# Performance work log

Measured on AMD Instinct MI355X. Metric: run time of the kernel, lower is better.

Reference implementation:

```python
import jax, jax.numpy as jnp
import numpy as np

B = 32          # batch size
N = 32          # image dim -> P = N*N points per sample
P = N * N
F = 64          # point feature dim (= MLP output)
K = 32          # max_neighbors
R = 0.1         # ball-query radius
EPS = 1e-5      # batchnorm eps


def setup_inputs() -> dict:
    key = jax.random.key(0)
    ks = jax.random.split(key, 4)
    NP = B * P
    x = jax.random.normal(ks[0], (NP, F), jnp.float32)
    pos = jax.random.uniform(ks[1], (NP, 2), jnp.float32)
    # module requires exactly N*N points per sample, sorted by batch
    batch = jnp.repeat(jnp.arange(B, dtype=jnp.int32), P)
    # MLP([66,128,64]) params: Linear->BN->ReLU->Linear
    W1 = jax.random.normal(ks[2], (F + 2, 128), jnp.float32) * (1.0 / np.sqrt(F + 2))
    b1 = jnp.zeros((128,), jnp.float32)
    gamma1 = jnp.ones((128,), jnp.float32)
    beta1 = jnp.zeros((128,), jnp.float32)
    W2 = jax.random.normal(ks[3], (128, F), jnp.float32) * (1.0 / np.sqrt(128))
    b2 = jnp.zeros((F,), jnp.float32)
    return {"x": x, "pos": pos, "batch": batch, "W1": W1, "b1": b1,
            "gamma1": gamma1, "beta1": beta1, "W2": W2, "b2": b2}


def reference(x, pos, batch, W1, b1, gamma1, beta1, W2, b2):
    NP = x.shape[0]
    posb = pos.reshape(B, P, 2)
    # pixel (target) index of every query point: batch*N*N + row*N + col
    rows = jnp.clip((pos[:, 1] * N).astype(jnp.int32), 0, N - 1)
    cols = jnp.clip((pos[:, 0] * N).astype(jnp.int32), 0, N - 1)
    pix = batch.astype(jnp.int32) * (N * N) + rows * N + cols          # [NP]
    # radius ball query within each batch sample (deterministic: nearest-K within R)
    d2 = jnp.sum((posb[:, :, None, :] - posb[:, None, :, :]) ** 2, -1)  # [B,P,P]
    d2 = jnp.where(d2 <= R * R, d2, jnp.inf)
    negd, nbr = jax.lax.top_k(-d2, K)                                   # [B,P,K]
    valid = jnp.isfinite(negd)
    src = (jnp.arange(B, dtype=jnp.int32)[:, None, None] * P + nbr).reshape(-1)  # [B*P*K]
    dst = jnp.broadcast_to(pix.reshape(B, P)[:, :, None], (B, P, K)).reshape(-1)
    mask = valid.reshape(-1) & (src != dst)          # remove_self_loops
    # PointNetConv message: concat(x_j, pos_j - pos_i); pos_i indexed by mapped target
    relpos = pos[src] - pos[dst]
    msg_nb = jnp.concatenate([x[src], relpos], -1)                    # [B*P*K, F+2]
    # add_self_loops: edge (i, i) for every node -> relpos = 0
    msg_self = jnp.concatenate([x, jnp.zeros_like(pos)], -1)          # [NP, F+2]
    msg = jnp.concatenate([msg_nb, msg_self], 0)
    m = jnp.concatenate([mask, jnp.ones((NP,), bool)], 0)
    tgt = jnp.concatenate([dst, jnp.arange(NP, dtype=jnp.int32)], 0)
    # MLP: Linear -> BatchNorm(training stats over valid messages) -> ReLU -> Linear
    z = msg @ W1 + b1
    mf = m.astype(z.dtype)[:, None]
    cnt = jnp.sum(mf)
    mean = jnp.sum(z * mf, 0, keepdims=True) / cnt
    var = jnp.sum(((z - mean) ** 2) * mf, 0, keepdims=True) / cnt
    h = jax.nn.relu((z - mean) / jnp.sqrt(var + EPS) * gamma1 + beta1)
    o = h @ W2 + b2                                                    # [M, F]
    # scatter-max aggregation into B*N*N pixel nodes (self loops make all nonempty)
    o = jnp.where(m[:, None], o, -jnp.inf)
    pixel_features = jax.ops.segment_max(o, tgt, num_segments=NP)
    images = pixel_features.reshape(B, N, N, F).transpose(0, 3, 1, 2)
    return images
```

## Files before the change

### kernel.cpp

```cpp
#include <hip/hip_runtime.h>
#include <hip/hip_bf16.h>
#include <hip/hip_fp16.h>
#include <math.h>


#define NPTS   32768
#define KNB    32
#define BN_EPS 1e-5f

#define WS_NBRS     0u
#define WS_NBRCNT   4194304u
#define WS_SCSH     4719616u
#define WS_W2B      4720640u
#define WS_PART     4737024u
#define WS_Y        5265408u
#define WS_SCRATCH  5265408u
#define WS_WB       13654016u
#define WS_QCNT     22042624u
#define WS_QSTART   22173696u
#define WS_QLIST    22304768u
#define WS_ISLOT    22435840u
#define WS_SELF     22566912u
#define WS_SHP      30955520u
#define WS_BQPART   22566912u

typedef __attribute__((ext_vector_type(8))) _Float16 half8;
typedef __attribute__((ext_vector_type(2))) _Float16 half2v;
typedef __attribute__((ext_vector_type(4))) float floatx4;

__device__ __forceinline__ unsigned short f2h_bits(float f) {
    _Float16 h = (_Float16)f;
    return *reinterpret_cast<unsigned short*>(&h);
}
__device__ __forceinline__ float bf_lo(unsigned int w) { return __uint_as_float(w << 16); }
__device__ __forceinline__ float bf_hi(unsigned int w) { return __uint_as_float(w & 0xffff0000u); }
__device__ __forceinline__ unsigned int pack_bf2(float lo, float hi) {
    __hip_bfloat162 hh = __float22bfloat162_rn(make_float2(lo, hi));
    return *reinterpret_cast<unsigned int*>(&hh);
}
__device__ __forceinline__ unsigned int pack_h2(float lo, float hi) {
    half2v hh = { (_Float16)lo, (_Float16)hi };
    return *reinterpret_cast<unsigned int*>(&hh);
}

union ShBQ {
    struct {
        float2 poss[1024];
        float accd[1024], accx[1024], accy[1024];
        unsigned long long cand[4][256];
    } bq;
    struct {
        int cntS[1024], preS[1024], offS[1024], pixOf[1024];
        int wtot[4];
    } pm;
};

__launch_bounds__(256)
__global__ void k_bq(const float* __restrict__ pos,
                     int* __restrict__ nbrs, int* __restrict__ nbr_cnt,
                     float* __restrict__ bqpart,
                     const float* __restrict__ W2, unsigned short* __restrict__ w2b,
                     int* __restrict__ qcnt, int* __restrict__ qstart,
                     int* __restrict__ qlist, int* __restrict__ islot) {
    __shared__ ShBQ sh;
    int tid = threadIdx.x;

    if (blockIdx.x < 32) {
        int s = blockIdx.x;
        int gt = s * 256 + tid;
        {
            int j  = gt & 7;
            int L  = (gt >> 3) & 63;
            int ks = (gt >> 9) & 3;
            int t4 = gt >> 11;
            int k = ks * 32 + (L >> 4) * 8 + j;
            int n = t4 * 16 + (L & 15);
            w2b[gt] = f2h_bits(W2[k * 64 + n]);
        }
        int base = s << 10;
        for (int i = tid; i < 1024; i += 256) sh.pm.cntS[i] = 0;
        __syncthreads();
        for (int ql = tid; ql < 1024; ql += 256) {
            float2 p = *(const float2*)&pos[2 * (base + ql)];
            int row = min(max((int)(p.y * 32.0f), 0), 31);
            int col = min(max((int)(p.x * 32.0f), 0), 31);
            int pixl = row * 32 + col;
            sh.pm.pixOf[ql] = pixl;
            atomicAdd(&sh.pm.cntS[pixl], 1);
        }
        __syncthreads();
        int a0 = sh.pm.cntS[4 * tid], a1 = sh.pm.cntS[4 * tid + 1];
        int a2 = sh.pm.cntS[4 * tid + 2], a3 = sh.pm.cntS[4 * tid + 3];
        int tsum = a0 + a1 + a2 + a3;
        int lane = tid & 63, wv = tid >> 6;
        int v = tsum;
        for (int o = 1; o < 64; o <<= 1) { int u = __shfl_up(v, o); if (lane >= o) v += u; }
        if (lane == 63) sh.pm.wtot[wv] = v;
        __syncthreads();
        int wbase = 0;
        for (int w = 0; w < wv; ++w) wbase += sh.pm.wtot[w];
        int excl = wbase + v - tsum;
        sh.pm.preS[4 * tid] = excl;
        sh.pm.preS[4 * tid + 1] = excl + a0;
        sh.pm.preS[4 * tid + 2] = excl + a0 + a1;
        sh.pm.preS[4 * tid + 3] = excl + a0 + a1 + a2;
        __syncthreads();
        for (int i = tid; i < 1024; i += 256) sh.pm.offS[i] = sh.pm.preS[i];
        __syncthreads();
        for (int ql = tid; ql < 1024; ql += 256) {
            int p = sh.pm.pixOf[ql];
            int slot = atomicAdd(&sh.pm.offS[p], 1);
            qlist[base + slot] = base + ql;
            islot[base + ql] = base + slot;
        }
        for (int i = tid; i < 1024; i += 256) {
            qcnt[base + i] = sh.pm.cntS[i];
            qstart[base + i] = base + sh.pm.preS[i];
        }
        return;
    }

    int bqid = blockIdx.x - 32;
    int wave = tid >> 6, lane = tid & 63;
    int s = bqid >> 5;
    int chunk = bqid & 31;
    int base = s << 10;
    for (int i = tid; i < 1024; i += 256) sh.bq.poss[i] = *(const float2*)&pos[2 * (base + i)];
    for (int i = tid; i < 1024; i += 256) { sh.bq.accd[i] = 0.0f; sh.bq.accx[i] = 0.0f; sh.bq.accy[i] = 0.0f; }
    __syncthreads();
    float2 pr[16];
#pragma unroll
    for (int k = 0; k < 16; ++k) pr[k] = sh.bq.poss[k * 64 + lane];
    unsigned long long lb = (1ull << lane) - 1ull;

    float aD = 0, aE = 0, aF = 0;
    for (int qi = 0; qi < 8; ++qi) {
        int ql = chunk * 32 + wave * 8 + qi;
        int q = base + ql;
        float2 qp = sh.bq.poss[ql];
        int row = min(max((int)(qp.y * 32.0f), 0), 31);
        int col = min(max((int)(qp.x * 32.0f), 0), 31);
        int pixl = row * 32 + col;
        float2 tp = sh.bq.poss[pixl];
        int cnt = 0;
        __builtin_amdgcn_wave_barrier();
#pragma unroll
        for (int k = 0; k < 16; ++k) {
            float dx = pr[k].x - qp.x, dy = pr[k].y - qp.y;
            float d2 = __fadd_rn(__fmul_rn(dx, dx), __fmul_rn(dy, dy));
            bool pred = (d2 <= 0.01f);
            unsigned long long mask = __ballot(pred);
            if (pred) {
                int slot = cnt + (int)__popcll(mask & lb);
                if (slot < 256)
                    sh.bq.cand[wave][slot] = ((unsigned long long)__float_as_uint(d2) << 32)
                                             | (unsigned int)(k * 64 + lane);
            }
            cnt += (int)__popcll(mask);
        }
        cnt = min(cnt, 256);
        __builtin_amdgcn_wave_barrier();
        int osel = 0;
        for (int cb = 0; cb < cnt; cb += 64) {
            int i = cb + lane;
            bool sel = false;
            int j = 0;
            if (i < cnt) {
                unsigned long long key = sh.bq.cand[wave][i];
                j = (int)(key & 0xffffffffu);
                if (cnt <= KNB) {
                    sel = (j != pixl);
                } else {
                    int rank = 0;
                    for (int t = 0; t < cnt; ++t) rank += (sh.bq.cand[wave][t] < key) ? 1 : 0;
                    sel = (rank < KNB) && (j != pixl);
                }
            }
            unsigned long long mask = __ballot(sel);
            if (sel) {
                int slot = osel + (int)__popcll(mask & lb);
                nbrs[q * KNB + slot] = base + j;
                float rx = sh.bq.poss[j].x - tp.x, ry = sh.bq.poss[j].y - tp.y;
                aD += rx * rx; aE += rx * ry; aF += ry * ry;
                atomicAdd(&sh.bq.accd[j], 1.0f);
                atomicAdd(&sh.bq.accx[j], tp.x);
                atomicAdd(&sh.bq.accy[j], tp.y);
            }
            osel += (int)__popcll(mask);
        }
        if (lane == 0) nbr_cnt[q] = osel;
    }
#pragma unroll
    for (int o = 1; o < 64; o <<= 1) {
        aD += __shfl_xor(aD, o); aE += __shfl_xor(aE, o); aF += __shfl_xor(aF, o);
    }
    __syncthreads();
    float* pb = &bqpart[bqid * 3076];
    for (int i = tid; i < 1024; i += 256) {
        pb[i] = sh.bq.accd[i]; pb[1024 + i] = sh.bq.accx[i]; pb[2048 + i] = sh.bq.accy[i];
    }
    if (tid == 0) { pb[3072] = aD; pb[3073] = aE; pb[3074] = aF; }
}

__launch_bounds__(512)
__global__ void k_y(const float* __restrict__ x, const float* __restrict__ W1,
                    const float* __restrict__ b1, const float* __restrict__ pos,
                    const float* __restrict__ bqpart,
                    unsigned int* __restrict__ yb, float* __restrict__ partials) {
    __shared__ float w1s[64 * 128];
    __shared__ float stage[8][512];
    __shared__ float lsum[515];
    __shared__ float degS[128], stxS[128], styS[128];
    int tid = threadIdx.x;
    int nblock = blockIdx.x * 128;
    for (int i = tid; i < 64 * 128; i += 512) w1s[i] = W1[i];
    for (int i = tid; i < 515; i += 512) lsum[i] = 0.0f;
    if (tid < 128) {
        int n = nblock + tid;
        int s = n >> 10, off = n & 1023;
        const float* pb = &bqpart[(s * 32) * 3076];
        float d = 0, xx = 0, yy = 0;
        for (int j = 0; j < 32; ++j) {
            d  += pb[j * 3076 + off];
            xx += pb[j * 3076 + 1024 + off];
            yy += pb[j * 3076 + 2048 + off];
        }
        degS[tid] = d; stxS[tid] = xx; styS[tid] = yy;
    }
    __syncthreads();
    int wave = tid >> 6, lane = tid & 63;
    int f0 = 2 * lane, f1 = 2 * lane + 1;
    float b10 = b1[f0], b11 = b1[f1];
    float* st = &stage[wave][0];
    float P0 = 0, Q0 = 0, R0 = 0, S0 = 0, P1 = 0, Q1 = 0, R1 = 0, S1 = 0;
    float sB = 0, sC = 0, sDeg = 0;

    for (int it = 0; it < 2; ++it) {
        int nbase = nblock + (wave * 2 + it) * 8;
        __builtin_amdgcn_wave_barrier();
#pragma unroll
        for (int mm = 0; mm < 8; ++mm)
            st[mm * 64 + lane] = x[(nbase + mm) * 64 + lane];
        __builtin_amdgcn_wave_barrier();
        float z0[8], z1[8];
#pragma unroll
        for (int mm = 0; mm < 8; ++mm) { z0[mm] = b10; z1[mm] = b11; }
        for (int k4 = 0; k4 < 16; ++k4) {
            float2 wv0 = *(const float2*)&w1s[(k4 * 4 + 0) * 128 + f0];
            float2 wv1 = *(const float2*)&w1s[(k4 * 4 + 1) * 128 + f0];
            float2 wv2 = *(const float2*)&w1s[(k4 * 4 + 2) * 128 + f0];
            float2 wv3 = *(const float2*)&w1s[(k4 * 4 + 3) * 128 + f0];
#pragma unroll
            for (int mm = 0; mm < 8; ++mm) {
                float4 mk = *(const float4*)&st[mm * 64 + k4 * 4];
                z0[mm] += mk.x * wv0.x + mk.y * wv1.x + mk.z * wv2.x + mk.w * wv3.x;
                z1[mm] += mk.x * wv0.y + mk.y * wv1.y + mk.z * wv2.y + mk.w * wv3.y;
            }
        }
#pragma unroll
        for (int mm = 0; mm < 8; ++mm) {
            int n = nbase + mm;
            int li = n - nblock;
            float dg = degS[li];
            float wgt = 1.0f + dg;
            float Bn = dg * pos[2 * n]     - stxS[li];
            float Cn = dg * pos[2 * n + 1] - styS[li];
            float a = z0[mm], bq = z1[mm];
            P0 += wgt * a;  Q0 += wgt * a * a;  R0 += a * Bn;  S0 += a * Cn;
            P1 += wgt * bq; Q1 += wgt * bq * bq; R1 += bq * Bn; S1 += bq * Cn;
            sB += Bn; sC += Cn; sDeg += dg;
            yb[n * 64 + lane] = pack_bf2(a, bq);
        }
        __builtin_amdgcn_wave_barrier();
    }
    atomicAdd(&lsum[f0], P0);        atomicAdd(&lsum[f1], P1);
    atomicAdd(&lsum[128 + f0], Q0);  atomicAdd(&lsum[128 + f1], Q1);
    atomicAdd(&lsum[256 + f0], R0);  atomicAdd(&lsum[256 + f1], R1);
    atomicAdd(&lsum[384 + f0], S0);  atomicAdd(&lsum[384 + f1], S1);
    if (lane == 0) {
        atomicAdd(&lsum[512], sB);
        atomicAdd(&lsum[513], sC);
        atomicAdd(&lsum[514], sDeg);
    }
    __syncthreads();
    for (int i = tid; i < 515; i += 512) partials[blockIdx.x * 516 + i] = lsum[i];
}

__global__ void k_finalize(const float* __restrict__ gamma, const float* __restrict__ beta,
                           const float* __restrict__ W1, const float* __restrict__ partials,
                           const float* __restrict__ bqpart, float* __restrict__ scsh) {
    __shared__ float red[515];
    __shared__ float sDEF[3];
    int tid = threadIdx.x;
    if (tid < 3) sDEF[tid] = 0.0f;
    for (int i = tid; i < 515; i += 256) {
        float s = 0;
        for (int b = 0; b < 256; ++b) s += partials[b * 516 + i];
        red[i] = s;
    }
    __syncthreads();
    {
        float td = 0, te = 0, tf = 0;
        for (int b = tid; b < 1024; b += 256) {
            const float* pb = &bqpart[b * 3076 + 3072];
            td += pb[0]; te += pb[1]; tf += pb[2];
        }
        atomicAdd(&sDEF[0], td); atomicAdd(&sDEF[1], te); atomicAdd(&sDEF[2], tf);
    }
    __syncthreads();
    if (tid < 128) {
        int f = tid;
        float P = red[f], Q = red[128 + f], R = red[256 + f], S = red[384 + f];
        float SB = red[512], SC = red[513], SDeg = red[514];
        float u = W1[8192 + f], v = W1[8320 + f];
        float cntv = 32768.0f + SDeg;
        float mean = (P + u * SB + v * SC) / cntv;
        float E2 = (Q + 2.0f * u * R + 2.0f * v * S
                    + u * u * sDEF[0] + 2.0f * u * v * sDEF[1] + v * v * sDEF[2]) / cntv;
        float var = E2 - mean * mean;
        float sc = gamma[f] / sqrtf(var + BN_EPS);
        scsh[f] = sc;
        scsh[128 + f] = beta[f] - mean * sc;
    }
}

__launch_bounds__(256)
__global__ void k_self(const unsigned int* __restrict__ yb, const float* __restrict__ pos,
                       const float* __restrict__ W1, const float* __restrict__ scsh,
                       const unsigned short* __restrict__ w2b, const float* __restrict__ b2,
                       const int* __restrict__ qcnt,
                       unsigned int* __restrict__ wbuf, unsigned int* __restrict__ shpbuf,
                       float* __restrict__ selfbuf, float* __restrict__ out) {
    __shared__ unsigned short hbuf[4][16 * 136];
    int tid = threadIdx.x, wave = tid >> 6, lane = tid & 63;
    unsigned short* hb = hbuf[wave];
    half8 bfrag[4][4];
#pragma unroll
    for (int t = 0; t < 4; ++t)
#pragma unroll
        for (int ks = 0; ks < 4; ++ks)
            bfrag[t][ks] = *(const half8*)&w2b[((t * 4 + ks) * 64 + lane) * 8];
    int f0 = 2 * lane;
    float sc0 = scsh[f0],     sh0 = scsh[128 + f0];
    float sc1 = scsh[f0 + 1], sh1 = scsh[129 + f0];
    float u0 = W1[8192 + f0], v0 = W1[8320 + f0];
    float u1 = W1[8193 + f0], v1 = W1[8321 + f0];
    float b2v0 = b2[(lane & 15)],      b2v1 = b2[16 + (lane & 15)];
    float b2v2 = b2[32 + (lane & 15)], b2v3 = b2[48 + (lane & 15)];

    int nbase = (blockIdx.x * 4 + wave) * 16;
#pragma unroll
    for (int c = 0; c < 2; ++c) {
        unsigned int yw[8];
#pragma unroll
        for (int j = 0; j < 8; ++j)
            yw[j] = yb[(nbase + c * 8 + j) * 64 + lane];
#pragma unroll
        for (int j = 0; j < 8; ++j) {
            int e = c * 8 + j;
            int nn = nbase + e;
            float y0 = bf_lo(yw[j]), y1 = bf_hi(yw[j]);
            float h0 = fmaxf(y0 * sc0 + sh0, 0.0f);
            float h1 = fmaxf(y1 * sc1 + sh1, 0.0f);
            *(unsigned int*)&hb[e * 136 + f0] = pack_h2(h0, h1);
            float px = pos[2 * nn], py = pos[2 * nn + 1];
            float ts0 = (px * u0 + py * v0) * sc0;
            float ts1 = (px * u1 + py * v1) * sc1;
            wbuf[nn * 64 + lane]   = pack_h2(y0 * sc0 + ts0, y1 * sc1 + ts1);
            shpbuf[nn * 64 + lane] = pack_h2(sh0 - ts0, sh1 - ts1);
        }
    }
    __builtin_amdgcn_wave_barrier();
    floatx4 acc0 = {0,0,0,0}, acc1 = {0,0,0,0}, acc2 = {0,0,0,0}, acc3 = {0,0,0,0};
#pragma unroll
    for (int ks = 0; ks < 4; ++ks) {
        half8 a = *(const half8*)&hb[(lane & 15) * 136 + ks * 32 + (lane >> 4) * 8];
        acc0 = __builtin_amdgcn_mfma_f32_16x16x32_f16(a, bfrag[0][ks], acc0, 0, 0, 0);
        acc1 = __builtin_amdgcn_mfma_f32_16x16x32_f16(a, bfrag[1][ks], acc1, 0, 0, 0);
        acc2 = __builtin_amdgcn_mfma_f32_16x16x32_f16(a, bfrag[2][ks], acc2, 0, 0, 0);
        acc3 = __builtin_amdgcn_mfma_f32_16x16x32_f16(a, bfrag[3][ks], acc3, 0, 0, 0);
    }
    int nrow = nbase + (lane >> 4) * 4;
#pragma unroll
    for (int r = 0; r < 4; ++r) {
        int n = nrow + r;
        float o0 = acc0[r] + b2v0, o1 = acc1[r] + b2v1;
        float o2 = acc2[r] + b2v2, o3 = acc3[r] + b2v3;
        selfbuf[n * 64 + (lane & 15)]      = o0;
        selfbuf[n * 64 + 16 + (lane & 15)] = o1;
        selfbuf[n * 64 + 32 + (lane & 15)] = o2;
        selfbuf[n * 64 + 48 + (lane & 15)] = o3;
        if (qcnt[n] == 0) {
            int obase = (n >> 10) * 65536 + (n & 1023);
            out[obase + ((lane & 15)) * 1024]      = o0;
            out[obase + (16 + (lane & 15)) * 1024] = o1;
            out[obase + (32 + (lane & 15)) * 1024] = o2;
            out[obase + (48 + (lane & 15)) * 1024] = o3;
        }
    }
}

__launch_bounds__(256)
__global__ void k_out(const unsigned int* __restrict__ wbuf,
                      const unsigned int* __restrict__ shpbuf,
                      const float* __restrict__ pos,
                      const unsigned short* __restrict__ w2b, const float* __restrict__ b2,
                      const int* __restrict__ nbrs, const int* __restrict__ nbr_cnt,
                      const int* __restrict__ islot, float* __restrict__ scratch) {
    int tid = threadIdx.x, wave = tid >> 6, lane = tid & 63;
    half8 bfrag[4][4];
#pragma unroll
    for (int t = 0; t < 4; ++t)
#pragma unroll
        for (int ks = 0; ks < 4; ++ks)
            bfrag[t][ks] = *(const half8*)&w2b[((t * 4 + ks) * 64 + lane) * 8];
    float b2l = b2[lane];
    int em = lane & 15;
    int koff = (lane >> 4) * 4;
    int wid = blockIdx.x * 4 + wave;

    for (int qi = 0; qi < 2; ++qi) {
        int q = wid * 2 + qi;
        int m = nbr_cnt[q];
        int b = q >> 10;
        float om0[4], om1[4], om2[4], om3[4];
#pragma unroll
        for (int r = 0; r < 4; ++r) { om0[r] = -INFINITY; om1[r] = -INFINITY; om2[r] = -INFINITY; om3[r] = -INFINITY; }
        float qx = pos[2 * q], qy = pos[2 * q + 1];
        int row = min(max((int)(qy * 32.0f), 0), 31);
        int col = min(max((int)(qx * 32.0f), 0), 31);
        int pixq = (b << 10) + row * 32 + col;

        if (m > 0) {
            uint4 sv[4];
#pragma unroll
            for (int ks = 0; ks < 4; ++ks)
                sv[ks] = *(const uint4*)&shpbuf[pixq * 64 + ks * 16 + koff];
            int nv = (lane < m) ? nbrs[q * KNB + lane] : 0;
            int src0 = __shfl(nv, em);
            int src1 = __shfl(nv, 16 + em);
            bool two = (m > 16);
            uint4 g0[4], g1[4];
            const unsigned int* wp0 = &wbuf[src0 * 64 + koff];
#pragma unroll
            for (int ks = 0; ks < 4; ++ks) g0[ks] = *(const uint4*)&wp0[ks * 16];
            if (two) {
                const unsigned int* wp1 = &wbuf[src1 * 64 + koff];
#pragma unroll
                for (int ks = 0; ks < 4; ++ks) g1[ks] = *(const uint4*)&wp1[ks * 16];
            }
            int rowb = (lane >> 4) * 4;
            {
                floatx4 a0 = {0,0,0,0}, a1 = {0,0,0,0}, a2 = {0,0,0,0}, a3 = {0,0,0,0};
#pragma unroll
                for (int ks = 0; ks < 4; ++ks) {
                    union { unsigned int u[4]; half8 h8; } af;
#pragma unroll
                    for (int qd = 0; qd < 4; ++qd) {
                        unsigned int wd = (qd == 0) ? g0[ks].x : (qd == 1) ? g0[ks].y : (qd == 2) ? g0[ks].z : g0[ks].w;
                        unsigned int sd = (qd == 0) ? sv[ks].x : (qd == 1) ? sv[ks].y : (qd == 2) ? sv[ks].z : sv[ks].w;
                        half2v wh = *reinterpret_cast<half2v*>(&wd);
                        half2v shh = *reinterpret_cast<half2v*>(&sd);
                        half2v zz = { (_Float16)0.0f, (_Float16)0.0f };
                        half2v hh = __builtin_elementwise_max(wh + shh, zz);
                        af.u[qd] = *reinterpret_cast<unsigned int*>(&hh);
                    }
                    a0 = __builtin_amdgcn_mfma_f32_16x16x32_f16(af.h8, bfrag[0][ks], a0, 0, 0, 0);
                    a1 = __builtin_amdgcn_mfma_f32_16x16x32_f16(af.h8, bfrag[1][ks], a1, 0, 0, 0);
                    a2 = __builtin_amdgcn_mfma_f32_16x16x32_f16(af.h8, bfrag[2][ks], a2, 0, 0, 0);
                    a3 = __builtin_amdgcn_mfma_f32_16x16x32_f16(af.h8, bfrag[3][ks], a3, 0, 0, 0);
                }
#pragma unroll
                for (int r = 0; r < 4; ++r) {
                    if (rowb + r < m) {
                        om0[r] = fmaxf(om0[r], a0[r]);
                        om1[r] = fmaxf(om1[r], a1[r]);
                        om2[r] = fmaxf(om2[r], a2[r]);
                        om3[r] = fmaxf(om3[r], a3[r]);
                    }
                }
            }
            if (two) {
                floatx4 a0 = {0,0,0,0}, a1 = {0,0,0,0}, a2 = {0,0,0,0}, a3 = {0,0,0,0};
#pragma unroll
                for (int ks = 0; ks < 4; ++ks) {
                    union { unsigned int u[4]; half8 h8; } af;
#pragma unroll
                    for (int qd = 0; qd < 4; ++qd) {
                        unsigned int wd = (qd == 0) ? g1[ks].x : (qd == 1) ? g1[ks].y : (qd == 2) ? g1[ks].z : g1[ks].w;
                        unsigned int sd = (qd == 0) ? sv[ks].x : (qd == 1) ? sv[ks].y : (qd == 2) ? sv[ks].z : sv[ks].w;
                        half2v wh = *reinterpret_cast<half2v*>(&wd);
                        half2v shh = *reinterpret_cast<half2v*>(&sd);
                        half2v zz = { (_Float16)0.0f, (_Float16)0.0f };
                        half2v hh = __builtin_elementwise_max(wh + shh, zz);
                        af.u[qd] = *reinterpret_cast<unsigned int*>(&hh);
                    }
                    a0 = __builtin_amdgcn_mfma_f32_16x16x32_f16(af.h8, bfrag[0][ks], a0, 0, 0, 0);
                    a1 = __builtin_amdgcn_mfma_f32_16x16x32_f16(af.h8, bfrag[1][ks], a1, 0, 0, 0);
                    a2 = __builtin_amdgcn_mfma_f32_16x16x32_f16(af.h8, bfrag[2][ks], a2, 0, 0, 0);
                    a3 = __builtin_amdgcn_mfma_f32_16x16x32_f16(af.h8, bfrag[3][ks], a3, 0, 0, 0);
                }
#pragma unroll
                for (int r = 0; r < 4; ++r) {
                    int e = 16 + rowb + r;
                    if (e < m) {
                        om0[r] = fmaxf(om0[r], a0[r]);
                        om1[r] = fmaxf(om1[r], a1[r]);
                        om2[r] = fmaxf(om2[r], a2[r]);
                        om3[r] = fmaxf(om3[r], a3[r]);
                    }
                }
            }
        }
        float w0 = fmaxf(fmaxf(om0[0], om0[1]), fmaxf(om0[2], om0[3]));
        float w1 = fmaxf(fmaxf(om1[0], om1[1]), fmaxf(om1[2], om1[3]));
        float w2 = fmaxf(fmaxf(om2[0], om2[1]), fmaxf(om2[2], om2[3]));
        float w3 = fmaxf(fmaxf(om3[0], om3[1]), fmaxf(om3[2], om3[3]));
        w0 = fmaxf(w0, __shfl_xor(w0, 16)); w0 = fmaxf(w0, __shfl_xor(w0, 32));
        w1 = fmaxf(w1, __shfl_xor(w1, 16)); w1 = fmaxf(w1, __shfl_xor(w1, 32));
        w2 = fmaxf(w2, __shfl_xor(w2, 16)); w2 = fmaxf(w2, __shfl_xor(w2, 32));
        w3 = fmaxf(w3, __shfl_xor(w3, 16)); w3 = fmaxf(w3, __shfl_xor(w3, 32));
        int g4 = lane >> 4;
        float vf = (g4 == 0) ? w0 : (g4 == 1) ? w1 : (g4 == 2) ? w2 : w3;
        vf += b2l;
        scratch[islot[q] * 64 + lane] = vf;
    }
}

__launch_bounds__(256)
__global__ void k_gather(const float* __restrict__ scratch, const float* __restrict__ selfbuf,
                         const int* __restrict__ qcnt, const int* __restrict__ qstart,
                         float* __restrict__ out) {
    int tid = threadIdx.x, wave = tid >> 6, lane = tid & 63;
    int n = blockIdx.x * 4 + wave;
    int c = qcnt[n];
    if (c == 0) return;
    int qs = qstart[n];
    float v = selfbuf[n * 64 + lane];
    for (int i = 0; i < c; ++i)
        v = fmaxf(v, scratch[(qs + i) * 64 + lane]);
    out[(n >> 10) * 65536 + lane * 1024 + (n & 1023)] = v;
}

extern "C" void kernel_launch(void* const* d_in, const int* in_sizes, int n_in,
                              void* d_out, int out_size, void* d_ws, size_t ws_size,
                              hipStream_t stream) {
    const float* x     = (const float*)d_in[0];
    const float* pos   = (const float*)d_in[1];
    const float* W1    = (const float*)d_in[3];
    const float* b1    = (const float*)d_in[4];
    const float* gamma = (const float*)d_in[5];
    const float* beta  = (const float*)d_in[6];
    const float* W2    = (const float*)d_in[7];
    const float* b2    = (const float*)d_in[8];
    float* out = (float*)d_out;
    char* ws = (char*)d_ws;
    int*   nbrs     = (int*)(ws + WS_NBRS);
    int*   nbr_cnt  = (int*)(ws + WS_NBRCNT);
    float* scsh     = (float*)(ws + WS_SCSH);
    unsigned short* w2b = (unsigned short*)(ws + WS_W2B);
    float* partials = (float*)(ws + WS_PART);
    unsigned int* yb = (unsigned int*)(ws + WS_Y);
    float* scratch  = (float*)(ws + WS_SCRATCH);
    unsigned int* wbuf = (unsigned int*)(ws + WS_WB);
    int* qcnt   = (int*)(ws + WS_QCNT);
    int* qstart = (int*)(ws + WS_QSTART);
    int* qlist  = (int*)(ws + WS_QLIST);
    int* islot  = (int*)(ws + WS_ISLOT);
    float* selfbuf = (float*)(ws + WS_SELF);
    unsigned int* shpbuf = (unsigned int*)(ws + WS_SHP);
    float* bqpart   = (float*)(ws + WS_BQPART);

    k_bq<<<1056, 256, 0, stream>>>(pos, nbrs, nbr_cnt, bqpart, W2, w2b,
                                   qcnt, qstart, qlist, islot);
    k_y<<<256, 512, 0, stream>>>(x, W1, b1, pos, bqpart, yb, partials);
    k_finalize<<<1, 256, 0, stream>>>(gamma, beta, W1, partials, bqpart, scsh);
    k_self<<<NPTS / 64, 256, 0, stream>>>(yb, pos, W1, scsh, w2b, b2, qcnt,
                                          wbuf, shpbuf, selfbuf, out);
    k_out<<<NPTS / 8, 256, 0, stream>>>(wbuf, shpbuf, pos, w2b, b2,
                                        nbrs, nbr_cnt, islot, scratch);
    k_gather<<<NPTS / 4, 256, 0, stream>>>(scratch, selfbuf, qcnt, qstart, out);
}
```

Measured before the change: 245.0 us.

## Swizzle block indices across XCDs and hoist k_out loads with branchless gathers

```diff
diff --git a/kernel.cpp b/kernel.cpp
--- a/kernel.cpp
+++ b/kernel.cpp
@@ -120,7 +120,8 @@
         return;
     }
 
-    int bqid = blockIdx.x - 32;
+    int bqphys = blockIdx.x - 32;
+    int bqid = (bqphys & 7) * 128 + (bqphys >> 3);
     int wave = tid >> 6, lane = tid & 63;
     int s = bqid >> 5;
     int chunk = bqid & 31;
@@ -188,6 +189,7 @@
             }
             osel += (int)__popcll(mask);
         }
+        if (lane >= osel && lane < KNB) nbrs[q * KNB + lane] = base;
         if (lane == 0) nbr_cnt[q] = osel;
     }
 #pragma unroll
@@ -212,7 +214,8 @@
     __shared__ float lsum[515];
     __shared__ float degS[128], stxS[128], styS[128];
     int tid = threadIdx.x;
-    int nblock = blockIdx.x * 128;
+    int vb = (blockIdx.x & 7) * 32 + (blockIdx.x >> 3);
+    int nblock = vb * 128;
     for (int i = tid; i < 64 * 128; i += 512) w1s[i] = W1[i];
     for (int i = tid; i < 515; i += 512) lsum[i] = 0.0f;
     if (tid < 128) {
@@ -348,7 +351,8 @@
     float b2v0 = b2[(lane & 15)],      b2v1 = b2[16 + (lane & 15)];
     float b2v2 = b2[32 + (lane & 15)], b2v3 = b2[48 + (lane & 15)];
 
-    int nbase = (blockIdx.x * 4 + wave) * 16;
+    int vb = (blockIdx.x & 7) * 64 + (blockIdx.x >> 3);
+    int nbase = (vb * 4 + wave) * 16;
 #pragma unroll
     for (int c = 0; c < 2; ++c) {
         unsigned int yw[8];
@@ -417,98 +421,113 @@
     float b2l = b2[lane];
     int em = lane & 15;
     int koff = (lane >> 4) * 4;
-    int wid = blockIdx.x * 4 + wave;
-
+    int vb = (blockIdx.x & 7) * 512 + (blockIdx.x >> 3);
+    int wid = vb * 4 + wave;
+    int q0 = wid * 2, q1 = q0 + 1;
+
+    int m0 = nbr_cnt[q0], m1 = nbr_cnt[q1];
+    int nv0 = nbrs[q0 * KNB + (lane & 31)];
+    int nv1 = nbrs[q1 * KNB + (lane & 31)];
+    float2 qp0 = *(const float2*)&pos[2 * q0];
+    float2 qp1 = *(const float2*)&pos[2 * q1];
+    int is0 = islot[q0], is1 = islot[q1];
+
+    int row0 = min(max((int)(qp0.y * 32.0f), 0), 31);
+    int col0 = min(max((int)(qp0.x * 32.0f), 0), 31);
+    int pixq0 = ((q0 >> 10) << 10) + row0 * 32 + col0;
+    int row1 = min(max((int)(qp1.y * 32.0f), 0), 31);
+    int col1 = min(max((int)(qp1.x * 32.0f), 0), 31);
+    int pixq1 = ((q1 >> 10) << 10) + row1 * 32 + col1;
+
+    uint4 sv0[4], sv1[4];
+#pragma unroll
+    for (int ks = 0; ks < 4; ++ks) {
+        sv0[ks] = *(const uint4*)&shpbuf[pixq0 * 64 + ks * 16 + koff];
+        sv1[ks] = *(const uint4*)&shpbuf[pixq1 * 64 + ks * 16 + koff];
+    }
+
+#pragma unroll
     for (int qi = 0; qi < 2; ++qi) {
-        int q = wid * 2 + qi;
-        int m = nbr_cnt[q];
-        int b = q >> 10;
+        int m   = qi ? m1 : m0;
+        int nv  = qi ? nv1 : nv0;
+        int isq = qi ? is1 : is0;
         float om0[4], om1[4], om2[4], om3[4];
 #pragma unroll
         for (int r = 0; r < 4; ++r) { om0[r] = -INFINITY; om1[r] = -INFINITY; om2[r] = -INFINITY; om3[r] = -INFINITY; }
-        float qx = pos[2 * q], qy = pos[2 * q + 1];
-        int row = min(max((int)(qy * 32.0f), 0), 31);
-        int col = min(max((int)(qx * 32.0f), 0), 31);
-        int pixq = (b << 10) + row * 32 + col;
-
-        if (m > 0) {
-            uint4 sv[4];
-#pragma unroll
-            for (int ks = 0; ks < 4; ++ks)
-                sv[ks] = *(const uint4*)&shpbuf[pixq * 64 + ks * 16 + koff];
-            int nv = (lane < m) ? nbrs[q * KNB + lane] : 0;
-            int src0 = __shfl(nv, em);
-            int src1 = __shfl(nv, 16 + em);
-            bool two = (m > 16);
-            uint4 g0[4], g1[4];
-            const unsigned int* wp0 = &wbuf[src0 * 64 + koff];
-#pragma unroll
-            for (int ks = 0; ks < 4; ++ks) g0[ks] = *(const uint4*)&wp0[ks * 16];
-            if (two) {
-                const unsigned int* wp1 = &wbuf[src1 * 64 + koff];
-#pragma unroll
-                for (int ks = 0; ks < 4; ++ks) g1[ks] = *(const uint4*)&wp1[ks * 16];
-            }
-            int rowb = (lane >> 4) * 4;
-            {
-                floatx4 a0 = {0,0,0,0}, a1 = {0,0,0,0}, a2 = {0,0,0,0}, a3 = {0,0,0,0};
-#pragma unroll
-                for (int ks = 0; ks < 4; ++ks) {
-                    union { unsigned int u[4]; half8 h8; } af;
-#pragma unroll
-                    for (int qd = 0; qd < 4; ++qd) {
-                        unsigned int wd = (qd == 0) ? g0[ks].x : (qd == 1) ? g0[ks].y : (qd == 2) ? g0[ks].z : g0[ks].w;
-                        unsigned int sd = (qd == 0) ? sv[ks].x : (qd == 1) ? sv[ks].y : (qd == 2) ? sv[ks].z : sv[ks].w;
-                        half2v wh = *reinterpret_cast<half2v*>(&wd);
-                        half2v shh = *reinterpret_cast<half2v*>(&sd);
-                        half2v zz = { (_Float16)0.0f, (_Float16)0.0f };
-                        half2v hh = __builtin_elementwise_max(wh + shh, zz);
-                        af.u[qd] = *reinterpret_cast<unsigned int*>(&hh);
-                    }
-                    a0 = __builtin_amdgcn_mfma_f32_16x16x32_f16(af.h8, bfrag[0][ks], a0, 0, 0, 0);
-                    a1 = __builtin_amdgcn_mfma_f32_16x16x32_f16(af.h8, bfrag[1][ks], a1, 0, 0, 0);
-                    a2 = __builtin_amdgcn_mfma_f32_16x16x32_f16(af.h8, bfrag[2][ks], a2, 0, 0, 0);
-                    a3 = __builtin_amdgcn_mfma_f32_16x16x32_f16(af.h8, bfrag[3][ks], a3, 0, 0, 0);
+
+        int src0 = __shfl(nv, em);
+        int src1 = __shfl(nv, 16 + em);
+        uint4 g0[4], g1[4];
+        const unsigned int* wp0 = &wbuf[src0 * 64 + koff];
+        const unsigned int* wp1 = &wbuf[src1 * 64 + koff];
+#pragma unroll
+        for (int ks = 0; ks < 4; ++ks) g0[ks] = *(const uint4*)&wp0[ks * 16];
+#pragma unroll
+        for (int ks = 0; ks < 4; ++ks) g1[ks] = *(const uint4*)&wp1[ks * 16];
+
+        int rowb = (lane >> 4) * 4;
+        {
+            floatx4 a0 = {0,0,0,0}, a1 = {0,0,0,0}, a2 = {0,0,0,0}, a3 = {0,0,0,0};
+#pragma unroll
+            for (int ks = 0; ks < 4; ++ks) {
+                union { unsigned int u[4]; half8 h8; } af;
+                uint4 gg = g0[ks];
+                uint4 ss = qi ? sv1[ks] : sv0[ks];
+#pragma unroll
+                for (int qd = 0; qd < 4; ++qd) {
+                    unsigned int wd = (qd == 0) ? gg.x : (qd == 1) ? gg.y : (qd == 2) ? gg.z : gg.w;
+                    unsigned int sd = (qd == 0) ? ss.x : (qd == 1) ? ss.y : (qd == 2) ? ss.z : ss.w;
+                    half2v wh = *reinterpret_cast<half2v*>(&wd);
+                    half2v shh = *reinterpret_cast<half2v*>(&sd);
+                    half2v zz = { (_Float16)0.0f, (_Float16)0.0f };
+                    half2v hh = __builtin_elementwise_max(wh + shh, zz);
+                    af.u[qd] = *reinterpret_cast<unsigned int*>(&hh);
                 }
-#pragma unroll
-                for (int r = 0; r < 4; ++r) {
-                    if (rowb + r < m) {
-                        om0[r] = fmaxf(om0[r], a0[r]);
-                        om1[r] = fmaxf(om1[r], a1[r]);
-                        om2[r] = fmaxf(om2[r], a2[r]);
-                        om3[r] = fmaxf(om3[r], a3[r]);
-                    }
+                a0 = __builtin_amdgcn_mfma_f32_16x16x32_f16(af.h8, bfrag[0][ks], a0, 0, 0, 0);
+                a1 = __builtin_amdgcn_mfma_f32_16x16x32_f16(af.h8, bfrag[1][ks], a1, 0, 0, 0);
+                a2 = __builtin_amdgcn_mfma_f32_16x16x32_f16(af.h8, bfrag[2][ks], a2, 0, 0, 0);
+                a3 = __builtin_amdgcn_mfma_f32_16x16x32_f16(af.h8, bfrag[3][ks], a3, 0, 0, 0);
+            }
+#pragma unroll
+            for (int r = 0; r < 4; ++r) {
+                if (rowb + r < m) {
+                    om0[r] = fmaxf(om0[r], a0[r]);
+                    om1[r] = fmaxf(om1[r], a1[r]);
+                    om2[r] = fmaxf(om2[r], a2[r]);
+                    om3[r] = fmaxf(om3[r], a3[r]);
                 }
             }
-            if (two) {
-                floatx4 a0 = {0,0,0,0}, a1 = {0,0,0,0}, a2 = {0,0,0,0}, a3 = {0,0,0,0};
-#pragma unroll
-                for (int ks = 0; ks < 4; ++ks) {
-                    union { unsigned int u[4]; half8 h8; } af;
-#pragma unroll
-                    for (int qd = 0; qd < 4; ++qd) {
-                        unsigned int wd = (qd == 0) ? g1[ks].x : (qd == 1) ? g1[ks].y : (qd == 2) ? g1[ks].z : g1[ks].w;
-                        unsigned int sd = (qd == 0) ? sv[ks].x : (qd == 1) ? sv[ks].y : (qd == 2) ? sv[ks].z : sv[ks].w;
-                        half2v wh = *reinterpret_cast<half2v*>(&wd);
-                        half2v shh = *reinterpret_cast<half2v*>(&sd);
-                        half2v zz = { (_Float16)0.0f, (_Float16)0.0f };
-                        half2v hh = __builtin_elementwise_max(wh + shh, zz);
-                        af.u[qd] = *reinterpret_cast<unsigned int*>(&hh);
-                    }
-                    a0 = __builtin_amdgcn_mfma_f32_16x16x32_f16(af.h8, bfrag[0][ks], a0, 0, 0, 0);
-                    a1 = __builtin_amdgcn_mfma_f32_16x16x32_f16(af.h8, bfrag[1][ks], a1, 0, 0, 0);
-                    a2 = __builtin_amdgcn_mfma_f32_16x16x32_f16(af.h8, bfrag[2][ks], a2, 0, 0, 0);
-                    a3 = __builtin_amdgcn_mfma_f32_16x16x32_f16(af.h8, bfrag[3][ks], a3, 0, 0, 0);
+        }
+        {
+            floatx4 a0 = {0,0,0,0}, a1 = {0,0,0,0}, a2 = {0,0,0,0}, a3 = {0,0,0,0};
+#pragma unroll
+            for (int ks = 0; ks < 4; ++ks) {
+                union { unsigned int u[4]; half8 h8; } af;
+                uint4 gg = g1[ks];
+                uint4 ss = qi ? sv1[ks] : sv0[ks];
+#pragma unroll
+                for (int qd = 0; qd < 4; ++qd) {
+                    unsigned int wd = (qd == 0) ? gg.x : (qd == 1) ? gg.y : (qd == 2) ? gg.z : gg.w;
+                    unsigned int sd = (qd == 0) ? ss.x : (qd == 1) ? ss.y : (qd == 2) ? ss.z : ss.w;
+                    half2v wh = *reinterpret_cast<half2v*>(&wd);
+                    half2v shh = *reinterpret_cast<half2v*>(&sd);
+                    half2v zz = { (_Float16)0.0f, (_Float16)0.0f };
+                    half2v hh = __builtin_elementwise_max(wh + shh, zz);
+                    af.u[qd] = *reinterpret_cast<unsigned int*>(&hh);
                 }
-#pragma unroll
-                for (int r = 0; r < 4; ++r) {
-                    int e = 16 + rowb + r;
-                    if (e < m) {
-                        om0[r] = fmaxf(om0[r], a0[r]);
-                        om1[r] = fmaxf(om1[r], a1[r]);
-                        om2[r] = fmaxf(om2[r], a2[r]);
-                        om3[r] = fmaxf(om3[r], a3[r]);
-                    }
+                a0 = __builtin_amdgcn_mfma_f32_16x16x32_f16(af.h8, bfrag[0][ks], a0, 0, 0, 0);
+                a1 = __builtin_amdgcn_mfma_f32_16x16x32_f16(af.h8, bfrag[1][ks], a1, 0, 0, 0);
+                a2 = __builtin_amdgcn_mfma_f32_16x16x32_f16(af.h8, bfrag[2][ks], a2, 0, 0, 0);
+                a3 = __builtin_amdgcn_mfma_f32_16x16x32_f16(af.h8, bfrag[3][ks], a3, 0, 0, 0);
+            }
+#pragma unroll
+            for (int r = 0; r < 4; ++r) {
+                int e = 16 + rowb + r;
+                if (e < m) {
+                    om0[r] = fmaxf(om0[r], a0[r]);
+                    om1[r] = fmaxf(om1[r], a1[r]);
+                    om2[r] = fmaxf(om2[r], a2[r]);
+                    om3[r] = fmaxf(om3[r], a3[r]);
                 }
             }
         }
@@ -523,7 +542,7 @@
         int g4 = lane >> 4;
         float vf = (g4 == 0) ? w0 : (g4 == 1) ? w1 : (g4 == 2) ? w2 : w3;
         vf += b2l;
-        scratch[islot[q] * 64 + lane] = vf;
+        scratch[isq * 64 + lane] = vf;
     }
 }
 
@@ -532,7 +551,8 @@
                          const int* __restrict__ qcnt, const int* __restrict__ qstart,
                          float* __restrict__ out) {
     int tid = threadIdx.x, wave = tid >> 6, lane = tid & 63;
-    int n = blockIdx.x * 4 + wave;
+    int vb = (blockIdx.x & 7) * 1024 + (blockIdx.x >> 3);
+    int n = vb * 4 + wave;
     int c = qcnt[n];
     if (c == 0) return;
     int qs = qstart[n];
```

After: 243.7 us. No clear change (-0.5%).
